# Performance work log

Measured on AMD Instinct MI355X. Metric: run time of the kernel, lower is better.

Reference implementation:

```python
import jax, jax.numpy as jnp
import numpy as np

BN_EPS = 1e-5
LEAKY_SLOPE = 0.2


def setup_inputs() -> dict:
    key = jax.random.key(0)
    B, T, J, H = 32, 128, 24, 256
    ks = jax.random.split(key, 16)

    def w(k, shape, scale=0.05):
        return jax.random.normal(k, shape, dtype=jnp.float32) * scale

    return {
        "xt_seq": jax.random.normal(ks[0], (B, T, J * 3), dtype=jnp.float32),
        "tau_seq": jax.random.uniform(ks[1], (B, T, 1), dtype=jnp.float32),
        "z_seq": jax.random.normal(ks[2], (B, T, H), dtype=jnp.float32),
        "h_n": jax.random.normal(ks[3], (1, B, H), dtype=jnp.float32),
        "adj": jax.random.uniform(ks[4], (J, J), dtype=jnp.float32),
        # linear weights stored as [in, out] (transposed vs torch)
        "w_joint": w(ks[5], (3, H)), "b_joint": jnp.zeros((H,), jnp.float32),
        "w_t1": w(ks[6], (1, H)), "b_t1": jnp.zeros((H,), jnp.float32),
        "w_t2": w(ks[7], (H, H)), "b_t2": jnp.zeros((H,), jnp.float32),
        "w_radar": w(ks[8], (H, H)), "b_radar": jnp.zeros((H,), jnp.float32),
        "w_gcn": w(ks[9], (H, H)), "b_gcn": jnp.zeros((H,), jnp.float32),
        "w_conv": w(ks[10], (H, H, 3)), "b_conv": jnp.zeros((H,), jnp.float32),  # [out,in,k]
        "bn_gamma": jnp.ones((H,), jnp.float32), "bn_beta": jnp.zeros((H,), jnp.float32),
        "bn_mean": jnp.zeros((H,), jnp.float32), "bn_var": jnp.ones((H,), jnp.float32),
        "w_out": w(ks[11], (H, 3)), "b_out": jnp.zeros((3,), jnp.float32),
    }


def _forward(xt_seq, tau_seq, z_seq, h_n, adj,
             w_joint, b_joint, w_t1, b_t1, w_t2, b_t2,
             w_radar, b_radar, w_gcn, b_gcn, w_conv, b_conv,
             bn_gamma, bn_beta, bn_mean, bn_var, w_out, b_out):
    B, T, _ = xt_seq.shape
    J = adj.shape[0]
    H = w_radar.shape[0]

    x = xt_seq.reshape(B, T, J, 3)
    h = x @ w_joint + b_joint                                  # [B,T,J,H]

    t_emb = jax.nn.silu(tau_seq @ w_t1 + b_t1) @ w_t2 + b_t2   # [B,T,H]
    h = h + t_emb[:, :, None, :]

    z_proj = z_seq @ w_radar + b_radar                         # [B,T,H]
    h = h + z_proj[:, :, None, :]

    h_radar = h_n[0] @ w_radar + b_radar                       # [B,H]
    h = h + h_radar[:, None, None, :]

    # GCN adjacency aggregation + linear + relu residual
    h_gcn = jnp.einsum('jk,btkh->btjh', adj, h)
    h = h + jax.nn.relu(h_gcn @ w_gcn + b_gcn)

    # temporal conv over T: [B*J, H, T]
    h_t = h.transpose(0, 2, 3, 1).reshape(B * J, H, T)
    h_t = jax.lax.conv_general_dilated(
        h_t, w_conv, window_strides=(1,), padding=[(1, 1)],
        dimension_numbers=('NCH', 'OIH', 'NCH')) + b_conv[None, :, None]
    # BatchNorm1d in eval mode (running stats)
    scale = bn_gamma * jax.lax.rsqrt(bn_var + BN_EPS)
    h_t = (h_t - bn_mean[None, :, None]) * scale[None, :, None] + bn_beta[None, :, None]
    h_t = jnp.where(h_t >= 0, h_t, LEAKY_SLOPE * h_t)

    h = h_t.reshape(B, J, H, T).transpose(0, 3, 1, 2)          # [B,T,J,H]
    v = h @ w_out + b_out                                      # [B,T,J,3]
    return v.reshape(B, T, -1)


def reference(xt_seq, tau_seq, z_seq, h_n, adj,
              w_joint, b_joint, w_t1, b_t1, w_t2, b_t2,
              w_radar, b_radar, w_gcn, b_gcn, w_conv, b_conv,
              bn_gamma, bn_beta, bn_mean, bn_var, w_out, b_out):
    return _forward(xt_seq, tau_seq, z_seq, h_n, adj,
                    w_joint, b_joint, w_t1, b_t1, w_t2, b_t2,
                    w_radar, b_radar, w_gcn, b_gcn, w_conv, b_conv,
                    bn_gamma, bn_beta, bn_mean, bn_var, w_out, b_out)
```

## Files before the change

### kernel.cpp

```cpp
#include <hip/hip_runtime.h>

typedef __attribute__((ext_vector_type(8))) short short8v;
typedef __attribute__((ext_vector_type(4))) float float4v;
typedef unsigned short u16;

constexpr int B_ = 32, T_ = 128, J_ = 24, H_ = 256;
constexpr int BT_ = B_ * T_;
constexpr int M_  = BT_ * J_;
constexpr float BN_EPS_ = 1e-5f, SLOPE_ = 0.2f;

constexpr size_t OB_HGB  = 0;
constexpr size_t OB_HB   = OB_HGB + (size_t)M_ * H_ * 2;
constexpr size_t OB_WTF  = OB_HB  + (size_t)M_ * H_ * 2;
constexpr size_t OB_WGF  = OB_WTF + 768 * 256 * 2;
constexpr size_t OB_BASE = OB_WGF + 256 * 256 * 2;
constexpr size_t OB_BNSC = OB_BASE + (size_t)BT_ * H_ * 4;
constexpr size_t OB_BNSH = OB_BNSC + 256 * 4;

__device__ __forceinline__ u16 f2b(float f) {
  union { float f; unsigned u; } v; v.f = f;
  return (u16)((v.u + 0x7fffu + ((v.u >> 16) & 1u)) >> 16);
}
__device__ __forceinline__ float b2f(u16 u) {
  union { unsigned u; float f; } v; v.u = ((unsigned)u) << 16; return v.f;
}

__global__ __launch_bounds__(256) void k_pack2(
    const float* __restrict__ w_conv, const float* __restrict__ w_gcn,
    const float* __restrict__ gamma, const float* __restrict__ beta,
    const float* __restrict__ mean, const float* __restrict__ var,
    u16* __restrict__ wtf, u16* __restrict__ wgf,
    float* __restrict__ bnsc, float* __restrict__ bnsh) {
  __shared__ float wlds[12288];
  int bid = blockIdx.x, tid = threadIdx.x;
  if (bid < 16) {
    int nblk = bid, o0 = nblk * 16;
#pragma unroll
    for (int p = 0; p < 12; ++p) {
      int lin = tid + p * 256;
      int row = lin / 192, c4 = lin % 192;
      *(float4*)&wlds[row * 768 + c4 * 4] =
          *(const float4*)&w_conv[(size_t)(o0 + row) * 768 + c4 * 4];
    }
    __syncthreads();
#pragma unroll
    for (int p = 0; p < 6; ++p) {
      int unit = tid + p * 256;
      int kb = unit >> 6, l = unit & 63;
      int col = l & 15, kb8 = (l >> 4) * 8;
      u16 tmp[8];
#pragma unroll
      for (int j = 0; j < 8; ++j) {
        int k = kb * 32 + kb8 + j;
        int tap = k >> 8, i = k & 255;
        tmp[j] = f2b(wlds[col * 768 + i * 3 + tap]);
      }
      *(short8v*)&wtf[((size_t)kb * 16 + nblk) * 512 + l * 8] = *(short8v*)tmp;
    }
  } else if (bid < 24) {
    int kb = bid - 16;
#pragma unroll
    for (int p = 0; p < 8; ++p) {
      int lin = tid + p * 256;
      int row = lin >> 6, c4 = lin & 63;
      *(float4*)&wlds[row * 256 + c4 * 4] =
          *(const float4*)&w_gcn[((size_t)kb * 32 + row) * 256 + c4 * 4];
    }
    __syncthreads();
#pragma unroll
    for (int p = 0; p < 4; ++p) {
      int unit = tid + p * 256;
      int nblk = unit >> 6, l = unit & 63;
      int col = l & 15, kb8 = (l >> 4) * 8;
      u16 tmp[8];
#pragma unroll
      for (int j = 0; j < 8; ++j)
        tmp[j] = f2b(wlds[(kb8 + j) * 256 + nblk * 16 + col]);
      *(short8v*)&wgf[((size_t)kb * 16 + nblk) * 512 + l * 8] = *(short8v*)tmp;
    }
  } else {
    float sc = gamma[tid] * rsqrtf(var[tid] + BN_EPS_);
    bnsc[tid] = sc;
    bnsh[tid] = beta[tid] - mean[tid] * sc;
  }
}

__global__ __launch_bounds__(256) void k_base2(
    const float* __restrict__ tau, const float* __restrict__ w_t1,
    const float* __restrict__ b_t1, const float* __restrict__ z,
    const float* __restrict__ hn, const float* __restrict__ w_t2,
    const float* __restrict__ w_radar, const float* __restrict__ b_t2,
    const float* __restrict__ b_radar, float* __restrict__ basep) {
  __shared__ float As[16][40];
  __shared__ float Bs[16][128];
  int bm = blockIdx.x & 127, bn = blockIdx.x >> 7;
  int row0 = bm * 32, col0 = bn * 128;
  int tid = threadIdx.x, ty = tid >> 5, tx = tid & 31;
  int sr = tid >> 2, sq = tid & 3;
  float tauv = (tid < 128) ? tau[row0 + sr] : 0.f;
  int bb = bm >> 2;
  float acc[4][4] = {};
  for (int ck = 0; ck < 32; ++ck) {
    int half = ck >> 4;
    int k0 = (ck & 15) * 16;
    if (tid < 128) {
      int kk4 = k0 + sq * 4;
      float4 v;
      if (half == 0) {
        float4 w1  = *(const float4*)&w_t1[kk4];
        float4 bb1 = *(const float4*)&b_t1[kk4];
        float t0 = tauv * w1.x + bb1.x, t1 = tauv * w1.y + bb1.y;
        float t2 = tauv * w1.z + bb1.z, t3 = tauv * w1.w + bb1.w;
        v.x = t0 / (1.f + expf(-t0)); v.y = t1 / (1.f + expf(-t1));
        v.z = t2 / (1.f + expf(-t2)); v.w = t3 / (1.f + expf(-t3));
      } else {
        float4 zv = *(const float4*)&z[(size_t)(row0 + sr) * 256 + kk4];
        float4 hv = *(const float4*)&hn[(size_t)bb * 256 + kk4];
        v = make_float4(zv.x + hv.x, zv.y + hv.y, zv.z + hv.z, zv.w + hv.w);
      }
      As[sq * 4 + 0][sr] = v.x; As[sq * 4 + 1][sr] = v.y;
      As[sq * 4 + 2][sr] = v.z; As[sq * 4 + 3][sr] = v.w;
    }
    const float* W = half ? w_radar : w_t2;
#pragma unroll
    for (int p = 0; p < 2; ++p) {
      int idx = tid + p * 256;
      int br = idx >> 5, c4 = idx & 31;
      *(float4*)&Bs[br][c4 * 4] = *(const float4*)&W[(size_t)(k0 + br) * 256 + col0 + c4 * 4];
    }
    __syncthreads();
#pragma unroll
    for (int kk = 0; kk < 16; ++kk) {
      float4 av = *(const float4*)&As[kk][ty * 4];
      float4 bv = *(const float4*)&Bs[kk][tx * 4];
      float a[4] = {av.x, av.y, av.z, av.w};
      float b[4] = {bv.x, bv.y, bv.z, bv.w};
#pragma unroll
      for (int i = 0; i < 4; ++i)
#pragma unroll
        for (int j = 0; j < 4; ++j) acc[i][j] += a[i] * b[j];
    }
    __syncthreads();
  }
#pragma unroll
  for (int i = 0; i < 4; ++i) {
    int bt = row0 + ty * 4 + i;
    int c = col0 + tx * 4;
    float4 o;
    o.x = acc[i][0] + b_t2[c + 0] + b_radar[c + 0];
    o.y = acc[i][1] + b_t2[c + 1] + b_radar[c + 1];
    o.z = acc[i][2] + b_t2[c + 2] + b_radar[c + 2];
    o.w = acc[i][3] + b_t2[c + 3] + b_radar[c + 3];
    *(float4*)&basep[(size_t)bt * 256 + c] = o;
  }
}

__global__ __launch_bounds__(256) void k_hg2(
    const float* __restrict__ xt, const float* __restrict__ basep,
    const float* __restrict__ adj, const float* __restrict__ w_joint,
    const float* __restrict__ b_joint, u16* __restrict__ hgb,
    u16* __restrict__ hb) {
  __shared__ float xs[72];
  __shared__ __align__(16) u16 stage[2][24][256];
  int bt = blockIdx.x, c = threadIdx.x;
  if (c < 18) ((float4*)xs)[c] = ((const float4*)(xt + (size_t)bt * 72))[c];
  __syncthreads();
  float wj0 = w_joint[c], wj1 = w_joint[256 + c], wj2 = w_joint[512 + c];
  float hbase = b_joint[c] + basep[(size_t)bt * 256 + c];
  float hv[24];
#pragma unroll
  for (int j = 0; j < 24; ++j) {
    hv[j] = xs[3 * j] * wj0 + xs[3 * j + 1] * wj1 + xs[3 * j + 2] * wj2 + hbase;
    stage[0][j][c] = f2b(hv[j]);
  }
  float ag[24] = {};
#pragma unroll
  for (int kp = 0; kp < 24; ++kp) {
    float av = hv[kp];
#pragma unroll
    for (int j = 0; j < 24; ++j) ag[j] += adj[j * 24 + kp] * av;
  }
#pragma unroll
  for (int j = 0; j < 24; ++j) stage[1][j][c] = f2b(ag[j]);
  __syncthreads();
  size_t gro = (size_t)bt * 24 * 256;
#pragma unroll
  for (int p = 0; p < 3; ++p) {
    int uu = c + p * 256;
    int j = uu >> 5, c8 = uu & 31;
    *(short8v*)&hb[gro + j * 256 + c8 * 8] = *(const short8v*)&stage[0][j][c8 * 8];
  }
#pragma unroll
  for (int p = 0; p < 3; ++p) {
    int uu = c + p * 256;
    int j = uu >> 5, c8 = uu & 31;
    *(short8v*)&hgb[gro + j * 256 + c8 * 8] = *(const short8v*)&stage[1][j][c8 * 8];
  }
}

#define DO_MFMA(A_, B_) do {                                              \
  _Pragma("unroll") for (int mi_ = 0; mi_ < 4; ++mi_)                     \
  _Pragma("unroll") for (int ni_ = 0; ni_ < 4; ++ni_)                     \
    acc[mi_][ni_] = __builtin_amdgcn_mfma_f32_16x16x32_bf16(              \
        A_[mi_], B_[ni_], acc[mi_][ni_], 0, 0, 0);                        \
} while (0)

__global__ __launch_bounds__(512, 2) void k_gcn4(
    const u16* __restrict__ wgf, const float* __restrict__ b_gcn,
    const u16* __restrict__ hb, u16* __restrict__ hgb) {
  __shared__ u16 Asm[128 * 256];
  int tid = threadIdx.x;
  int l = tid & 63, w = tid >> 6;
  int wm = w >> 2, wn = w & 3;
  int l15 = l & 15, hi16 = (l >> 4) * 16, l8 = l * 8;
  int bid = blockIdx.x;
  int swz = (bid & 7) * 96 + (bid >> 3);
  int r0 = swz * 128;
  char* ab = (char*)Asm;

#pragma unroll
  for (int p = 0; p < 8; ++p) {
    int c = tid + p * 512;
    int lr = c >> 5, c16 = c & 31;
    short8v v = *(const short8v*)&hgb[(size_t)(r0 + lr) * 256 + c16 * 8];
    int off = (lr * 512 + c16 * 16) ^ ((lr & 7) << 4);
    *(short8v*)(ab + off) = v;
  }
  __syncthreads();

  float4v z4 = {0.f, 0.f, 0.f, 0.f};
  float4v acc[4][4];
#pragma unroll
  for (int mi = 0; mi < 4; ++mi)
#pragma unroll
    for (int ni = 0; ni < 4; ++ni) acc[mi][ni] = z4;

  const u16* wbase = wgf + (size_t)wn * 4 * 512 + l8;

#define LB_G(dst, kb) do {                                                \
  const u16* bp_ = wbase + (size_t)(kb) * 16 * 512;                       \
  _Pragma("unroll") for (int ni_ = 0; ni_ < 4; ++ni_)                     \
    dst[ni_] = *(const short8v*)(bp_ + ni_ * 512);                        \
} while (0)
#define LA_G(dst, kb) do {                                                \
  _Pragma("unroll") for (int mi_ = 0; mi_ < 4; ++mi_) {                   \
    int lr_ = wm * 64 + mi_ * 16 + l15;                                   \
    int off_ = (lr_ * 512 + (kb) * 64 + hi16) ^ ((lr_ & 7) << 4);         \
    dst[mi_] = *(const short8v*)(ab + off_);                              \
  }                                                                       \
} while (0)

  short8v a0[4], a1[4], b0[4], b1[4];
  LB_G(b0, 0); LB_G(b1, 1); LA_G(a0, 0); LA_G(a1, 1);
#pragma unroll
  for (int kb2 = 0; kb2 < 8; kb2 += 2) {
    DO_MFMA(a0, b0);
    if (kb2 + 2 < 8) { LB_G(b0, kb2 + 2); LA_G(a0, kb2 + 2); }
    DO_MFMA(a1, b1);
    if (kb2 + 3 < 8) { LB_G(b1, kb2 + 3); LA_G(a1, kb2 + 3); }
  }
#undef LB_G
#undef LA_G

  int g = l >> 4;
#pragma unroll
  for (int ni = 0; ni < 4; ++ni) {
    int col = wn * 64 + ni * 16 + l15;
    float bg = b_gcn[col];
#pragma unroll
    for (int mi = 0; mi < 4; ++mi)
#pragma unroll
      for (int r = 0; r < 4; ++r) {
        int row = r0 + wm * 64 + mi * 16 + g * 4 + r;
        float hres = b2f(hb[(size_t)row * 256 + col]);
        float gv = acc[mi][ni][r] + bg;
        hgb[(size_t)row * 256 + col] = f2b(hres + (gv > 0.f ? gv : 0.f));
      }
  }
}

__global__ __launch_bounds__(512, 2) void k_conv4(
    const u16* __restrict__ wtf, const float* __restrict__ b_conv,
    const float* __restrict__ bnsc, const float* __restrict__ bnsh,
    const float* __restrict__ w_out, const float* __restrict__ b_out,
    const u16* __restrict__ h2b, float* __restrict__ vout) {
  __shared__ u16 Asm[176 * 256];
  __shared__ float pvbuf[4][128][3];
  int tid = threadIdx.x;
  int l = tid & 63, w = tid >> 6;
  int wm = w >> 2, wn = w & 3;
  int l15 = l & 15, hi16 = (l >> 4) * 16, l8 = l * 8;
  int bid = blockIdx.x;
  int swz = (bid & 7) * 96 + (bid >> 3);
  int r0 = swz * 128;
  char* ab = (char*)Asm;

#pragma unroll
  for (int p = 0; p < 11; ++p) {
    int c = tid + p * 512;
    int lr = c >> 5, c16 = c & 31;
    int grow = r0 - 24 + lr;
    grow = grow < 0 ? 0 : (grow >= M_ ? M_ - 1 : grow);
    short8v v = *(const short8v*)&h2b[(size_t)grow * 256 + c16 * 8];
    int off = (lr * 512 + c16 * 16) ^ ((lr & 7) << 4);
    *(short8v*)(ab + off) = v;
  }
  __syncthreads();

  int t0[4];
#pragma unroll
  for (int mi = 0; mi < 4; ++mi) {
    int row = r0 + wm * 64 + mi * 16 + l15;
    t0[mi] = (row / 24) & 127;
  }
  short8v z8 = {0, 0, 0, 0, 0, 0, 0, 0};

  float4v z4 = {0.f, 0.f, 0.f, 0.f};
  float4v acc[4][4];
#pragma unroll
  for (int mi = 0; mi < 4; ++mi)
#pragma unroll
    for (int ni = 0; ni < 4; ++ni) acc[mi][ni] = z4;

  const u16* wbase = wtf + (size_t)wn * 4 * 512 + l8;

#define LB_C(dst, kb) do {                                                \
  const u16* bp_ = wbase + (size_t)(kb) * 16 * 512;                       \
  _Pragma("unroll") for (int ni_ = 0; ni_ < 4; ++ni_)                     \
    dst[ni_] = *(const short8v*)(bp_ + ni_ * 512);                        \
} while (0)
#define LA_C(dst, kb) do {                                                \
  int tap_ = (kb) >> 3;                                                   \
  _Pragma("unroll") for (int mi_ = 0; mi_ < 4; ++mi_) {                   \
    int lr_ = tap_ * 24 + wm * 64 + mi_ * 16 + l15;                       \
    int off_ = (lr_ * 512 + ((kb) & 7) * 64 + hi16) ^ ((lr_ & 7) << 4);   \
    short8v v_ = *(const short8v*)(ab + off_);                            \
    if (tap_ != 1) {                                                      \
      bool ok_ = (unsigned)(t0[mi_] + tap_ - 1) < 128u;                   \
      v_ = ok_ ? v_ : z8;                                                 \
    }                                                                     \
    dst[mi_] = v_;                                                        \
  }                                                                       \
} while (0)

  short8v A2[2][4], Bq[4][4];
  LB_C(Bq[0], 0); LB_C(Bq[1], 1); LB_C(Bq[2], 2); LB_C(Bq[3], 3);
  LA_C(A2[0], 0); LA_C(A2[1], 1);
#pragma unroll
  for (int kb = 0; kb < 24; ++kb) {
    DO_MFMA(A2[kb & 1], Bq[kb & 3]);
    if (kb + 4 < 24) LB_C(Bq[kb & 3], kb + 4);
    if (kb + 2 < 24) LA_C(A2[kb & 1], kb + 2);
  }
#undef LB_C
#undef LA_C

  float pv[4][4][3] = {};
#pragma unroll
  for (int ni = 0; ni < 4; ++ni) {
    int col = wn * 64 + ni * 16 + l15;
    float bc = b_conv[col], scv = bnsc[col], shv = bnsh[col];
    float w0v = w_out[col * 3], w1v = w_out[col * 3 + 1], w2v = w_out[col * 3 + 2];
#pragma unroll
    for (int mi = 0; mi < 4; ++mi)
#pragma unroll
      for (int r = 0; r < 4; ++r) {
        float hv = acc[mi][ni][r] + bc;
        hv = hv * scv + shv;
        hv = (hv >= 0.f) ? hv : SLOPE_ * hv;
        pv[mi][r][0] += hv * w0v;
        pv[mi][r][1] += hv * w1v;
        pv[mi][r][2] += hv * w2v;
      }
  }
#pragma unroll
  for (int mi = 0; mi < 4; ++mi)
#pragma unroll
    for (int r = 0; r < 4; ++r)
#pragma unroll
      for (int c = 0; c < 3; ++c) {
        float v = pv[mi][r][c];
        v += __shfl_xor(v, 1);
        v += __shfl_xor(v, 2);
        v += __shfl_xor(v, 4);
        v += __shfl_xor(v, 8);
        pv[mi][r][c] = v;
      }
  int g = l >> 4;
  if (l15 == 0) {
#pragma unroll
    for (int mi = 0; mi < 4; ++mi)
#pragma unroll
      for (int r = 0; r < 4; ++r) {
        int rl = wm * 64 + mi * 16 + g * 4 + r;
        pvbuf[wn][rl][0] = pv[mi][r][0];
        pvbuf[wn][rl][1] = pv[mi][r][1];
        pvbuf[wn][rl][2] = pv[mi][r][2];
      }
  }
  __syncthreads();
  if (tid < 384) {
    int row = tid / 3, c = tid - row * 3;
    float sum = pvbuf[0][row][c] + pvbuf[1][row][c] + pvbuf[2][row][c] +
                pvbuf[3][row][c] + b_out[c];
    vout[(size_t)(r0 + row) * 3 + c] = sum;
  }
}

extern "C" void kernel_launch(void* const* d_in, const int* in_sizes, int n_in,
                              void* d_out, int out_size, void* d_ws, size_t ws_size,
                              hipStream_t stream) {
  (void)in_sizes; (void)n_in; (void)out_size; (void)ws_size;
  const float* xt      = (const float*)d_in[0];
  const float* tau     = (const float*)d_in[1];
  const float* z       = (const float*)d_in[2];
  const float* hn      = (const float*)d_in[3];
  const float* adj     = (const float*)d_in[4];
  const float* w_joint = (const float*)d_in[5];
  const float* b_joint = (const float*)d_in[6];
  const float* w_t1    = (const float*)d_in[7];
  const float* b_t1    = (const float*)d_in[8];
  const float* w_t2    = (const float*)d_in[9];
  const float* b_t2    = (const float*)d_in[10];
  const float* w_radar = (const float*)d_in[11];
  const float* b_radar = (const float*)d_in[12];
  const float* w_gcn   = (const float*)d_in[13];
  const float* b_gcn   = (const float*)d_in[14];
  const float* w_conv  = (const float*)d_in[15];
  const float* b_conv  = (const float*)d_in[16];
  const float* gamma   = (const float*)d_in[17];
  const float* beta    = (const float*)d_in[18];
  const float* mean    = (const float*)d_in[19];
  const float* var     = (const float*)d_in[20];
  const float* w_out   = (const float*)d_in[21];
  const float* b_out   = (const float*)d_in[22];

  char* wsb = (char*)d_ws;
  u16*   hgb   = (u16*)(wsb + OB_HGB);
  u16*   hbres = (u16*)(wsb + OB_HB);
  u16*   wtf   = (u16*)(wsb + OB_WTF);
  u16*   wgf   = (u16*)(wsb + OB_WGF);
  float* basep = (float*)(wsb + OB_BASE);
  float* bnsc  = (float*)(wsb + OB_BNSC);
  float* bnsh  = (float*)(wsb + OB_BNSH);
  float* vout  = (float*)d_out;

  hipLaunchKernelGGL(k_pack2, dim3(25), dim3(256), 0, stream,
                     w_conv, w_gcn, gamma, beta, mean, var, wtf, wgf, bnsc, bnsh);
  hipLaunchKernelGGL(k_base2, dim3(256), dim3(256), 0, stream,
                     tau, w_t1, b_t1, z, hn, w_t2, w_radar, b_t2, b_radar, basep);
  hipLaunchKernelGGL(k_hg2, dim3(BT_), dim3(256), 0, stream,
                     xt, basep, adj, w_joint, b_joint, hgb, hbres);
  hipLaunchKernelGGL(k_gcn4, dim3(M_ / 128), dim3(512), 0, stream,
                     wgf, b_gcn, hbres, hgb);
  hipLaunchKernelGGL(k_conv4, dim3(M_ / 128), dim3(512), 0, stream,
                     wtf, b_conv, bnsc, bnsh, w_out, b_out, hgb, vout);
}
```

Measured before the change: 274.3 us.

## Fuse GCN linear into conv kernel and recompute residual instead of storing it

Merges the GCN GEMM and the temporal conv GEMM into one kernel. Each block recomputes the GCN output for its 128 rows plus a 24-row halo on each side (192 rows), directly in LDS. The pre-GCN residual h is recomputed from xt, w_joint and basep instead of being written to and read back from a separate buffer. This removes one full bf16 intermediate round trip to global memory and one kernel launch. The cost is redundant GCN work on halo rows, higher register and LDS use, and occupancy dropping to one block per CU.

```diff
diff --git a/kernel.cpp b/kernel.cpp
--- a/kernel.cpp
+++ b/kernel.cpp
@@ -10,8 +10,7 @@
 constexpr float BN_EPS_ = 1e-5f, SLOPE_ = 0.2f;
 
 constexpr size_t OB_HGB  = 0;
-constexpr size_t OB_HB   = OB_HGB + (size_t)M_ * H_ * 2;
-constexpr size_t OB_WTF  = OB_HB  + (size_t)M_ * H_ * 2;
+constexpr size_t OB_WTF  = OB_HGB + (size_t)M_ * H_ * 2;
 constexpr size_t OB_WGF  = OB_WTF + 768 * 256 * 2;
 constexpr size_t OB_BASE = OB_WGF + 256 * 256 * 2;
 constexpr size_t OB_BNSC = OB_BASE + (size_t)BT_ * H_ * 4;
@@ -20,9 +19,6 @@
 __device__ __forceinline__ u16 f2b(float f) {
   union { float f; unsigned u; } v; v.f = f;
   return (u16)((v.u + 0x7fffu + ((v.u >> 16) & 1u)) >> 16);
-}
-__device__ __forceinline__ float b2f(u16 u) {
-  union { unsigned u; float f; } v; v.u = ((unsigned)u) << 16; return v.f;
 }
 
 __global__ __launch_bounds__(256) void k_pack2(
@@ -155,13 +151,12 @@
   }
 }
 
-__global__ __launch_bounds__(256) void k_hg2(
+__global__ __launch_bounds__(256) void k_hg3(
     const float* __restrict__ xt, const float* __restrict__ basep,
     const float* __restrict__ adj, const float* __restrict__ w_joint,
-    const float* __restrict__ b_joint, u16* __restrict__ hgb,
-    u16* __restrict__ hb) {
+    const float* __restrict__ b_joint, u16* __restrict__ hgb) {
   __shared__ float xs[72];
-  __shared__ __align__(16) u16 stage[2][24][256];
+  __shared__ __align__(16) u16 stage[24][256];
   int bt = blockIdx.x, c = threadIdx.x;
   if (c < 18) ((float4*)xs)[c] = ((const float4*)(xt + (size_t)bt * 72))[c];
   __syncthreads();
@@ -169,10 +164,8 @@
   float hbase = b_joint[c] + basep[(size_t)bt * 256 + c];
   float hv[24];
 #pragma unroll
-  for (int j = 0; j < 24; ++j) {
+  for (int j = 0; j < 24; ++j)
     hv[j] = xs[3 * j] * wj0 + xs[3 * j + 1] * wj1 + xs[3 * j + 2] * wj2 + hbase;
-    stage[0][j][c] = f2b(hv[j]);
-  }
   float ag[24] = {};
 #pragma unroll
   for (int kp = 0; kp < 24; ++kp) {
@@ -181,129 +174,134 @@
     for (int j = 0; j < 24; ++j) ag[j] += adj[j * 24 + kp] * av;
   }
 #pragma unroll
-  for (int j = 0; j < 24; ++j) stage[1][j][c] = f2b(ag[j]);
+  for (int j = 0; j < 24; ++j) stage[j][c] = f2b(ag[j]);
   __syncthreads();
   size_t gro = (size_t)bt * 24 * 256;
 #pragma unroll
   for (int p = 0; p < 3; ++p) {
     int uu = c + p * 256;
     int j = uu >> 5, c8 = uu & 31;
-    *(short8v*)&hb[gro + j * 256 + c8 * 8] = *(const short8v*)&stage[0][j][c8 * 8];
-  }
-#pragma unroll
-  for (int p = 0; p < 3; ++p) {
-    int uu = c + p * 256;
-    int j = uu >> 5, c8 = uu & 31;
-    *(short8v*)&hgb[gro + j * 256 + c8 * 8] = *(const short8v*)&stage[1][j][c8 * 8];
-  }
-}
-
-#define DO_MFMA(A_, B_) do {                                              \
-  _Pragma("unroll") for (int mi_ = 0; mi_ < 4; ++mi_)                     \
-  _Pragma("unroll") for (int ni_ = 0; ni_ < 4; ++ni_)                     \
-    acc[mi_][ni_] = __builtin_amdgcn_mfma_f32_16x16x32_bf16(              \
-        A_[mi_], B_[ni_], acc[mi_][ni_], 0, 0, 0);                        \
-} while (0)
-
-__global__ __launch_bounds__(512, 2) void k_gcn4(
-    const u16* __restrict__ wgf, const float* __restrict__ b_gcn,
-    const u16* __restrict__ hb, u16* __restrict__ hgb) {
-  __shared__ u16 Asm[128 * 256];
-  int tid = threadIdx.x;
-  int l = tid & 63, w = tid >> 6;
-  int wm = w >> 2, wn = w & 3;
-  int l15 = l & 15, hi16 = (l >> 4) * 16, l8 = l * 8;
-  int bid = blockIdx.x;
-  int swz = (bid & 7) * 96 + (bid >> 3);
-  int r0 = swz * 128;
-  char* ab = (char*)Asm;
-
-#pragma unroll
-  for (int p = 0; p < 8; ++p) {
-    int c = tid + p * 512;
-    int lr = c >> 5, c16 = c & 31;
-    short8v v = *(const short8v*)&hgb[(size_t)(r0 + lr) * 256 + c16 * 8];
-    int off = (lr * 512 + c16 * 16) ^ ((lr & 7) << 4);
-    *(short8v*)(ab + off) = v;
-  }
-  __syncthreads();
-
-  float4v z4 = {0.f, 0.f, 0.f, 0.f};
-  float4v acc[4][4];
-#pragma unroll
-  for (int mi = 0; mi < 4; ++mi)
-#pragma unroll
-    for (int ni = 0; ni < 4; ++ni) acc[mi][ni] = z4;
-
-  const u16* wbase = wgf + (size_t)wn * 4 * 512 + l8;
-
-#define LB_G(dst, kb) do {                                                \
-  const u16* bp_ = wbase + (size_t)(kb) * 16 * 512;                       \
-  _Pragma("unroll") for (int ni_ = 0; ni_ < 4; ++ni_)                     \
-    dst[ni_] = *(const short8v*)(bp_ + ni_ * 512);                        \
-} while (0)
-#define LA_G(dst, kb) do {                                                \
-  _Pragma("unroll") for (int mi_ = 0; mi_ < 4; ++mi_) {                   \
-    int lr_ = wm * 64 + mi_ * 16 + l15;                                   \
-    int off_ = (lr_ * 512 + (kb) * 64 + hi16) ^ ((lr_ & 7) << 4);         \
-    dst[mi_] = *(const short8v*)(ab + off_);                              \
-  }                                                                       \
-} while (0)
-
-  short8v a0[4], a1[4], b0[4], b1[4];
-  LB_G(b0, 0); LB_G(b1, 1); LA_G(a0, 0); LA_G(a1, 1);
-#pragma unroll
-  for (int kb2 = 0; kb2 < 8; kb2 += 2) {
-    DO_MFMA(a0, b0);
-    if (kb2 + 2 < 8) { LB_G(b0, kb2 + 2); LA_G(a0, kb2 + 2); }
-    DO_MFMA(a1, b1);
-    if (kb2 + 3 < 8) { LB_G(b1, kb2 + 3); LA_G(a1, kb2 + 3); }
-  }
-#undef LB_G
-#undef LA_G
-
-  int g = l >> 4;
-#pragma unroll
-  for (int ni = 0; ni < 4; ++ni) {
-    int col = wn * 64 + ni * 16 + l15;
-    float bg = b_gcn[col];
-#pragma unroll
-    for (int mi = 0; mi < 4; ++mi)
-#pragma unroll
-      for (int r = 0; r < 4; ++r) {
-        int row = r0 + wm * 64 + mi * 16 + g * 4 + r;
-        float hres = b2f(hb[(size_t)row * 256 + col]);
-        float gv = acc[mi][ni][r] + bg;
-        hgb[(size_t)row * 256 + col] = f2b(hres + (gv > 0.f ? gv : 0.f));
-      }
-  }
-}
-
-__global__ __launch_bounds__(512, 2) void k_conv4(
-    const u16* __restrict__ wtf, const float* __restrict__ b_conv,
+    *(short8v*)&hgb[gro + j * 256 + c8 * 8] = *(const short8v*)&stage[j][c8 * 8];
+  }
+}
+
+__global__ __launch_bounds__(512, 1) void k_mega(
+    const u16* __restrict__ wgf, const u16* __restrict__ wtf,
+    const float* __restrict__ b_gcn, const float* __restrict__ xt,
+    const float* __restrict__ basep, const float* __restrict__ w_joint,
+    const float* __restrict__ b_joint, const float* __restrict__ b_conv,
     const float* __restrict__ bnsc, const float* __restrict__ bnsh,
     const float* __restrict__ w_out, const float* __restrict__ b_out,
-    const u16* __restrict__ h2b, float* __restrict__ vout) {
-  __shared__ u16 Asm[176 * 256];
+    const u16* __restrict__ hgb, float* __restrict__ vout) {
+  __shared__ u16 Asm[192 * 256];
   __shared__ float pvbuf[4][128][3];
   int tid = threadIdx.x;
   int l = tid & 63, w = tid >> 6;
   int wm = w >> 2, wn = w & 3;
   int l15 = l & 15, hi16 = (l >> 4) * 16, l8 = l * 8;
+  int g = l >> 4;
   int bid = blockIdx.x;
   int swz = (bid & 7) * 96 + (bid >> 3);
   int r0 = swz * 128;
   char* ab = (char*)Asm;
 
 #pragma unroll
-  for (int p = 0; p < 11; ++p) {
+  for (int p = 0; p < 12; ++p) {
     int c = tid + p * 512;
     int lr = c >> 5, c16 = c & 31;
     int grow = r0 - 24 + lr;
     grow = grow < 0 ? 0 : (grow >= M_ ? M_ - 1 : grow);
-    short8v v = *(const short8v*)&h2b[(size_t)grow * 256 + c16 * 8];
+    short8v v = *(const short8v*)&hgb[(size_t)grow * 256 + c16 * 8];
     int off = (lr * 512 + c16 * 16) ^ ((lr & 7) << 4);
     *(short8v*)(ab + off) = v;
+  }
+  __syncthreads();
+
+  float4v z4 = {0.f, 0.f, 0.f, 0.f};
+  float4v accg[6][4];
+#pragma unroll
+  for (int mi = 0; mi < 6; ++mi)
+#pragma unroll
+    for (int ni = 0; ni < 4; ++ni) accg[mi][ni] = z4;
+
+  const u16* wb_g = wgf + (size_t)wn * 4 * 512 + l8;
+
+#define LBG(dst, kb) do {                                                 \
+  const u16* bp_ = wb_g + (size_t)(kb) * 16 * 512;                        \
+  _Pragma("unroll") for (int ni_ = 0; ni_ < 4; ++ni_)                     \
+    dst[ni_] = *(const short8v*)(bp_ + ni_ * 512);                        \
+} while (0)
+#define LAG(dst, kb) do {                                                 \
+  _Pragma("unroll") for (int mi_ = 0; mi_ < 6; ++mi_) {                   \
+    int lr_ = wm * 96 + mi_ * 16 + l15;                                   \
+    int off_ = (lr_ * 512 + (kb) * 64 + hi16) ^ ((lr_ & 7) << 4);         \
+    dst[mi_] = *(const short8v*)(ab + off_);                              \
+  }                                                                       \
+} while (0)
+#define MFMA6(A_, B_) do {                                                \
+  _Pragma("unroll") for (int mi_ = 0; mi_ < 6; ++mi_)                     \
+  _Pragma("unroll") for (int ni_ = 0; ni_ < 4; ++ni_)                     \
+    accg[mi_][ni_] = __builtin_amdgcn_mfma_f32_16x16x32_bf16(             \
+        A_[mi_], B_[ni_], accg[mi_][ni_], 0, 0, 0);                       \
+} while (0)
+
+  {
+    short8v ag0[6], ag1[6], bg0[4], bg1[4];
+    LBG(bg0, 0); LBG(bg1, 1); LAG(ag0, 0); LAG(ag1, 1);
+#pragma unroll
+    for (int kb2 = 0; kb2 < 8; kb2 += 2) {
+      MFMA6(ag0, bg0);
+      if (kb2 + 2 < 8) { LBG(bg0, kb2 + 2); LAG(ag0, kb2 + 2); }
+      MFMA6(ag1, bg1);
+      if (kb2 + 3 < 8) { LBG(bg1, kb2 + 3); LAG(ag1, kb2 + 3); }
+    }
+  }
+#undef LBG
+#undef LAG
+#undef MFMA6
+
+  __syncthreads();
+
+  const u16* wb_c = wtf + (size_t)wn * 4 * 512 + l8;
+#define LBC(dst, kb) do {                                                 \
+  const u16* bp_ = wb_c + (size_t)(kb) * 16 * 512;                        \
+  _Pragma("unroll") for (int ni_ = 0; ni_ < 4; ++ni_)                     \
+    dst[ni_] = *(const short8v*)(bp_ + ni_ * 512);                        \
+} while (0)
+  short8v Bq[4][4];
+  LBC(Bq[0], 0); LBC(Bq[1], 1); LBC(Bq[2], 2); LBC(Bq[3], 3);
+
+  {
+    float wjc0[4], wjc1[4], wjc2[4], bjc[4], bgc[4];
+#pragma unroll
+    for (int ni = 0; ni < 4; ++ni) {
+      int col = wn * 64 + ni * 16 + l15;
+      wjc0[ni] = w_joint[col]; wjc1[ni] = w_joint[256 + col];
+      wjc2[ni] = w_joint[512 + col];
+      bjc[ni] = b_joint[col]; bgc[ni] = b_gcn[col];
+    }
+#pragma unroll
+    for (int mi = 0; mi < 6; ++mi)
+#pragma unroll
+      for (int r = 0; r < 4; ++r) {
+        int lrow = wm * 96 + mi * 16 + g * 4 + r;
+        int grow = r0 - 24 + lrow;
+        int growc = grow < 0 ? 0 : (grow >= M_ ? M_ - 1 : grow);
+        int bt = growc / 24;
+        float x0 = xt[(size_t)growc * 3 + 0];
+        float x1 = xt[(size_t)growc * 3 + 1];
+        float x2 = xt[(size_t)growc * 3 + 2];
+#pragma unroll
+        for (int ni = 0; ni < 4; ++ni) {
+          int col = wn * 64 + ni * 16 + l15;
+          float basev = basep[(size_t)bt * 256 + col];
+          float h = x0 * wjc0[ni] + x1 * wjc1[ni] + x2 * wjc2[ni] + bjc[ni] + basev;
+          float gv = accg[mi][ni][r] + bgc[ni];
+          float h2 = h + (gv > 0.f ? gv : 0.f);
+          int off = (lrow * 512 + col * 2) ^ ((lrow & 7) << 4);
+          *(u16*)(ab + off) = f2b(h2);
+        }
+      }
   }
   __syncthreads();
 
@@ -314,22 +312,13 @@
     t0[mi] = (row / 24) & 127;
   }
   short8v z8 = {0, 0, 0, 0, 0, 0, 0, 0};
-
-  float4v z4 = {0.f, 0.f, 0.f, 0.f};
-  float4v acc[4][4];
+  float4v accc[4][4];
 #pragma unroll
   for (int mi = 0; mi < 4; ++mi)
 #pragma unroll
-    for (int ni = 0; ni < 4; ++ni) acc[mi][ni] = z4;
-
-  const u16* wbase = wtf + (size_t)wn * 4 * 512 + l8;
-
-#define LB_C(dst, kb) do {                                                \
-  const u16* bp_ = wbase + (size_t)(kb) * 16 * 512;                       \
-  _Pragma("unroll") for (int ni_ = 0; ni_ < 4; ++ni_)                     \
-    dst[ni_] = *(const short8v*)(bp_ + ni_ * 512);                        \
-} while (0)
-#define LA_C(dst, kb) do {                                                \
+    for (int ni = 0; ni < 4; ++ni) accc[mi][ni] = z4;
+
+#define LAC(dst, kb) do {                                                 \
   int tap_ = (kb) >> 3;                                                   \
   _Pragma("unroll") for (int mi_ = 0; mi_ < 4; ++mi_) {                   \
     int lr_ = tap_ * 24 + wm * 64 + mi_ * 16 + l15;                       \
@@ -342,18 +331,26 @@
     dst[mi_] = v_;                                                        \
   }                                                                       \
 } while (0)
-
-  short8v A2[2][4], Bq[4][4];
-  LB_C(Bq[0], 0); LB_C(Bq[1], 1); LB_C(Bq[2], 2); LB_C(Bq[3], 3);
-  LA_C(A2[0], 0); LA_C(A2[1], 1);
-#pragma unroll
-  for (int kb = 0; kb < 24; ++kb) {
-    DO_MFMA(A2[kb & 1], Bq[kb & 3]);
-    if (kb + 4 < 24) LB_C(Bq[kb & 3], kb + 4);
-    if (kb + 2 < 24) LA_C(A2[kb & 1], kb + 2);
-  }
-#undef LB_C
-#undef LA_C
+#define MFMA4(A_, B_) do {                                                \
+  _Pragma("unroll") for (int mi_ = 0; mi_ < 4; ++mi_)                     \
+  _Pragma("unroll") for (int ni_ = 0; ni_ < 4; ++ni_)                     \
+    accc[mi_][ni_] = __builtin_amdgcn_mfma_f32_16x16x32_bf16(             \
+        A_[mi_], B_[ni_], accc[mi_][ni_], 0, 0, 0);                       \
+} while (0)
+
+  {
+    short8v A2[2][4];
+    LAC(A2[0], 0); LAC(A2[1], 1);
+#pragma unroll
+    for (int kb = 0; kb < 24; ++kb) {
+      MFMA4(A2[kb & 1], Bq[kb & 3]);
+      if (kb + 4 < 24) LBC(Bq[kb & 3], kb + 4);
+      if (kb + 2 < 24) LAC(A2[kb & 1], kb + 2);
+    }
+  }
+#undef LAC
+#undef LBC
+#undef MFMA4
 
   float pv[4][4][3] = {};
 #pragma unroll
@@ -365,7 +362,7 @@
     for (int mi = 0; mi < 4; ++mi)
 #pragma unroll
       for (int r = 0; r < 4; ++r) {
-        float hv = acc[mi][ni][r] + bc;
+        float hv = accc[mi][ni][r] + bc;
         hv = hv * scv + shv;
         hv = (hv >= 0.f) ? hv : SLOPE_ * hv;
         pv[mi][r][0] += hv * w0v;
@@ -386,7 +383,6 @@
         v += __shfl_xor(v, 8);
         pv[mi][r][c] = v;
       }
-  int g = l >> 4;
   if (l15 == 0) {
 #pragma unroll
     for (int mi = 0; mi < 4; ++mi)
@@ -437,7 +433,6 @@
 
   char* wsb = (char*)d_ws;
   u16*   hgb   = (u16*)(wsb + OB_HGB);
-  u16*   hbres = (u16*)(wsb + OB_HB);
   u16*   wtf   = (u16*)(wsb + OB_WTF);
   u16*   wgf   = (u16*)(wsb + OB_WGF);
   float* basep = (float*)(wsb + OB_BASE);
@@ -449,10 +444,9 @@
                      w_conv, w_gcn, gamma, beta, mean, var, wtf, wgf, bnsc, bnsh);
   hipLaunchKernelGGL(k_base2, dim3(256), dim3(256), 0, stream,
                      tau, w_t1, b_t1, z, hn, w_t2, w_radar, b_t2, b_radar, basep);
-  hipLaunchKernelGGL(k_hg2, dim3(BT_), dim3(256), 0, stream,
-                     xt, basep, adj, w_joint, b_joint, hgb, hbres);
-  hipLaunchKernelGGL(k_gcn4, dim3(M_ / 128), dim3(512), 0, stream,
-                     wgf, b_gcn, hbres, hgb);
-  hipLaunchKernelGGL(k_conv4, dim3(M_ / 128), dim3(512), 0, stream,
-                     wtf, b_conv, bnsc, bnsh, w_out, b_out, hgb, vout);
-}
+  hipLaunchKernelGGL(k_hg3, dim3(BT_), dim3(256), 0, stream,
+                     xt, basep, adj, w_joint, b_joint, hgb);
+  hipLaunchKernelGGL(k_mega, dim3(M_ / 128), dim3(512), 0, stream,
+                     wgf, wtf, b_gcn, xt, basep, w_joint, b_joint,
+                     b_conv, bnsc, bnsh, w_out, b_out, hgb, vout);
+}
```

Measured after the change: 266.5 us. -2.8%, faster.
